# Optimization experiments

Hardware: AMD Instinct MI355X
Metric: run time of the kernel (lower is better)

The kernel has to match this reference:

```python
import jax, jax.numpy as jnp
import numpy as np

T = 100          # number of landscape sample points
K_MAX = 2        # landscape depth
GRID = (256, 256)
N = GRID[0] * GRID[1]
B = 256          # batch size
P = 1024         # persistence pairs per sample (from the cubical complex)
DIMENSIONS = (0, 1)
BIG = jnp.float32(1e30)  # finite sentinel instead of inf (avoids inf arithmetic)


def setup_inputs() -> dict:
    key = jax.random.key(0)
    k1, k2, k3, k4 = jax.random.split(key, 4)
    inputs = jax.random.uniform(k1, (B, N), dtype=jnp.float32)
    dim_idx = jax.random.randint(k2, (B, P), 0, 2, dtype=jnp.int32)
    b_loc = jax.random.randint(k3, (B, P), 0, N, dtype=jnp.int32)
    d_loc = jax.random.randint(k4, (B, P), 0, N, dtype=jnp.int32)
    # persistence pairs satisfy death value >= birth value; swap to honor that
    vb = jnp.take_along_axis(inputs, b_loc, axis=1)
    vd = jnp.take_along_axis(inputs, d_loc, axis=1)
    swap = vb > vd
    birth_loc = jnp.where(swap, d_loc, b_loc)
    death_loc = jnp.where(swap, b_loc, d_loc)
    return {"inputs": inputs, "dim_idx": dim_idx,
            "birth_loc": birth_loc, "death_loc": death_loc}


def _landscape_sample(dtm, dim_idx, b_loc, d_loc):
    # dtm: [N] filtration values; pairs: [P] each
    births = dtm[b_loc]  # [P] birth value = input at birth cell
    deaths = dtm[d_loc]  # [P]
    lands, trange = [], []
    for dim in DIMENSIONS:
        valid = dim_idx == dim                     # [P] pairs of this homology dim
        count = jnp.sum(valid)
        # robust t-range: first K_MAX valid pairs in given (lexsort) order
        rank = jnp.cumsum(valid.astype(jnp.int32)) - 1
        sel = valid & (rank < K_MAX)
        t_min = jnp.min(jnp.where(sel, births, BIG))
        t_max = jnp.max(jnp.where(sel, deaths, -BIG))
        t_min = jnp.where(count > 0, t_min, 0.0)
        t_max = jnp.where(count > 0, t_max, 0.0)
        # original custom grad does NOT differentiate through tseq
        tseq = jax.lax.stop_gradient(jnp.linspace(t_min, t_max, T))  # [T]
        b = jnp.where(valid, births, BIG)
        d = jnp.where(valid, deaths, -BIG)
        # tent functions: [T, P]
        fab = jnp.maximum(jnp.minimum(tseq[:, None] - b[None, :],
                                      d[None, :] - tseq[:, None]), 0.0)
        land, _ = jax.lax.top_k(fab, K_MAX)        # == -sort(-fab)[:, :K_MAX]
        land = jnp.where(count > 0, land, jnp.zeros_like(land))
        nonzero = (count > 0) & (jnp.max(land) > 0)
        trange.append(jnp.where(nonzero, t_min, 0.0))
        trange.append(jnp.where(nonzero, t_max, 0.0))
        lands.append(land)
    return jnp.stack(lands), jax.lax.stop_gradient(jnp.stack(trange))


def reference(inputs, dim_idx, birth_loc, death_loc):
    # landscape: [B, len(DIMENSIONS), T, K_MAX]; t_range: [B, 2*len(DIMENSIONS)]
    land, t_range = jax.vmap(_landscape_sample)(inputs, dim_idx, birth_loc, death_loc)
    return land, t_range
```

## Files before the change

### kernel.cpp

```cpp
#include <hip/hip_runtime.h>

#define TT 100
#define PP 1024
#define NN 65536
#define BIGV 1e30f

__global__ __launch_bounds__(1024, 8) void adpl_kernel(
    const float* __restrict__ inputs,
    const int*   __restrict__ dim_idx,
    const int*   __restrict__ birth_loc,
    const int*   __restrict__ death_loc,
    float*       __restrict__ out_land,
    float*       __restrict__ out_trange)
{
    __shared__ float2 bd[PP];
    __shared__ unsigned long long s_mask[16];
    __shared__ float  s_tmin, s_tmax;
    __shared__ int    s_count;
    __shared__ int    s_maxland;
    __shared__ float2 s_part[TT][33];

    const int b   = blockIdx.x;
    const int d   = blockIdx.y;
    const int tid = threadIdx.x;

    if (tid == 0) s_maxland = 0;

    {
        const int p  = tid;
        const int di = dim_idx[(size_t)b * PP + p];
        const bool v = (di == d);
        float bv = BIGV, dv = -BIGV;
        if (v) {
            const int bl = birth_loc[(size_t)b * PP + p];
            const int dl = death_loc[(size_t)b * PP + p];
            bv = inputs[(size_t)b * NN + bl];
            dv = inputs[(size_t)b * NN + dl];
        }
        bd[p] = make_float2(bv, dv);
        const unsigned long long m = __ballot(v);
        if ((tid & 63) == 0) s_mask[tid >> 6] = m;
    }
    __syncthreads();

    if (tid == 0) {
        int cnt = 0, p1 = -1, p2 = -1;
        for (int w = 0; w < 16; w++) {
            unsigned long long m = s_mask[w];
            cnt += __popcll(m);
            if (p2 < 0 && m) {
                if (p1 < 0) {
                    p1 = w * 64 + __ffsll(m) - 1;
                    m &= m - 1;
                    if (m) p2 = w * 64 + __ffsll(m) - 1;
                } else {
                    p2 = w * 64 + __ffsll(m) - 1;
                }
            }
        }
        float tmin = 0.f, tmax = 0.f;
        if (cnt > 0) {
            const float2 e1 = bd[p1];
            tmin = e1.x; tmax = e1.y;
            if (cnt > 1) {
                const float2 e2 = bd[p2];
                tmin = fminf(tmin, e2.x);
                tmax = fmaxf(tmax, e2.y);
            }
        }
        s_tmin = tmin; s_tmax = tmax; s_count = cnt;
    }
    __syncthreads();

    if (tid < 800) {
        const int tg = tid >> 5;
        const int c  = tid & 31;
        const float tmin = s_tmin, tmax = s_tmax;
        const float step = (tmax - tmin) * (1.0f / (TT - 1));
        float tv[4], m1[4], m2[4];
        #pragma unroll
        for (int j = 0; j < 4; j++) {
            const int t = 4 * tg + j;
            tv[j] = (t == TT - 1) ? tmax : fmaf((float)t, step, tmin);
            m1[j] = 0.f; m2[j] = 0.f;
        }
        #pragma unroll 8
        for (int i = 0; i < 32; i++) {
            const float2 e = bd[32 * i + c];
            #pragma unroll
            for (int j = 0; j < 4; j++) {
                const float f = fminf(tv[j] - e.x, e.y - tv[j]);
                m2[j] = fmaxf(m2[j], fminf(m1[j], f));
                m1[j] = fmaxf(m1[j], f);
            }
        }
        #pragma unroll
        for (int j = 0; j < 4; j++)
            s_part[4 * tg + j][c] = make_float2(m1[j], m2[j]);
    }
    __syncthreads();

    if (tid < TT) {
        const int t = tid;
        float m1 = 0.f, m2 = 0.f;
        #pragma unroll 8
        for (int c = 0; c < 32; c++) {
            const float2 pr = s_part[t][c];
            m2 = fmaxf(fminf(m1, pr.x), fmaxf(m2, pr.y));
            m1 = fmaxf(m1, pr.x);
        }
        const size_t base = ((size_t)(b * 2 + d) * TT + t) * 2;
        *reinterpret_cast<float2*>(out_land + base) = make_float2(m1, m2);
        atomicMax(&s_maxland, __float_as_int(m1));
    }
    __syncthreads();

    if (tid == 0) {
        const bool nz = (s_count > 0) && (__int_as_float(s_maxland) > 0.f);
        const float tmn = nz ? s_tmin : 0.f;
        const float tmx = nz ? s_tmax : 0.f;
        *reinterpret_cast<float2*>(out_trange + (size_t)b * 4 + 2 * d) =
            make_float2(tmn, tmx);
    }
}

extern "C" void kernel_launch(void* const* d_in, const int* in_sizes, int n_in,
                              void* d_out, int out_size, void* d_ws, size_t ws_size,
                              hipStream_t stream) {
    const float* inputs    = (const float*)d_in[0];
    const int*   dim_idx   = (const int*)d_in[1];
    const int*   birth_loc = (const int*)d_in[2];
    const int*   death_loc = (const int*)d_in[3];

    const int B = in_sizes[1] / PP;

    float* out_land   = (float*)d_out;
    float* out_trange = out_land + (size_t)B * 2 * TT * 2;

    dim3 grid(B, 2);
    adpl_kernel<<<grid, 1024, 0, stream>>>(inputs, dim_idx, birth_loc, death_loc,
                                           out_land, out_trange);
}
```

Before: 106.6 us.

## Compact valid pairs in shared memory and scan only the valid count

```diff
diff --git a/kernel.cpp b/kernel.cpp
--- a/kernel.cpp
+++ b/kernel.cpp
@@ -13,69 +13,62 @@
     float*       __restrict__ out_land,
     float*       __restrict__ out_trange)
 {
-    __shared__ float2 bd[PP];
+    __shared__ float2 bd[PP + 32];
     __shared__ unsigned long long s_mask[16];
-    __shared__ float  s_tmin, s_tmax;
-    __shared__ int    s_count;
+    __shared__ float2 s_part[TT][33];
     __shared__ int    s_maxland;
-    __shared__ float2 s_part[TT][33];
 
-    const int b   = blockIdx.x;
-    const int d   = blockIdx.y;
-    const int tid = threadIdx.x;
+    const int b    = blockIdx.x;
+    const int d    = blockIdx.y;
+    const int tid  = threadIdx.x;
+    const int wave = tid >> 6;
+    const int lane = tid & 63;
 
     if (tid == 0) s_maxland = 0;
 
-    {
-        const int p  = tid;
-        const int di = dim_idx[(size_t)b * PP + p];
-        const bool v = (di == d);
-        float bv = BIGV, dv = -BIGV;
-        if (v) {
-            const int bl = birth_loc[(size_t)b * PP + p];
-            const int dl = death_loc[(size_t)b * PP + p];
-            bv = inputs[(size_t)b * NN + bl];
-            dv = inputs[(size_t)b * NN + dl];
-        }
-        bd[p] = make_float2(bv, dv);
-        const unsigned long long m = __ballot(v);
-        if ((tid & 63) == 0) s_mask[tid >> 6] = m;
+    const int di = dim_idx  [(size_t)b * PP + tid];
+    const int bl = birth_loc[(size_t)b * PP + tid];
+    const int dl = death_loc[(size_t)b * PP + tid];
+    const bool v = (di == d);
+    float bv = 0.f, dv = 0.f;
+    if (v) {
+        bv = inputs[(size_t)b * NN + bl];
+        dv = inputs[(size_t)b * NN + dl];
     }
+    const unsigned long long m = __ballot(v);
+    if (lane == 0) s_mask[wave] = m;
     __syncthreads();
 
-    if (tid == 0) {
-        int cnt = 0, p1 = -1, p2 = -1;
-        for (int w = 0; w < 16; w++) {
-            unsigned long long m = s_mask[w];
-            cnt += __popcll(m);
-            if (p2 < 0 && m) {
-                if (p1 < 0) {
-                    p1 = w * 64 + __ffsll(m) - 1;
-                    m &= m - 1;
-                    if (m) p2 = w * 64 + __ffsll(m) - 1;
-                } else {
-                    p2 = w * 64 + __ffsll(m) - 1;
-                }
-            }
+    int cnt = 0, base = 0;
+    #pragma unroll
+    for (int w = 0; w < 16; w++) {
+        const int pc = __popcll(s_mask[w]);
+        cnt  += pc;
+        base += (w < wave) ? pc : 0;
+    }
+    if (v) {
+        const int prefix = __popcll(m & ((1ull << lane) - 1ull));
+        bd[base + prefix] = make_float2(bv, dv);
+    }
+    const int cnt_pad = (cnt + 31) & ~31;
+    if (tid < cnt_pad - cnt)
+        bd[cnt + tid] = make_float2(BIGV, -BIGV);
+    __syncthreads();
+
+    float tmin = 0.f, tmax = 0.f;
+    if (cnt > 0) {
+        const float2 e1 = bd[0];
+        tmin = e1.x; tmax = e1.y;
+        if (cnt > 1) {
+            const float2 e2 = bd[1];
+            tmin = fminf(tmin, e2.x);
+            tmax = fmaxf(tmax, e2.y);
         }
-        float tmin = 0.f, tmax = 0.f;
-        if (cnt > 0) {
-            const float2 e1 = bd[p1];
-            tmin = e1.x; tmax = e1.y;
-            if (cnt > 1) {
-                const float2 e2 = bd[p2];
-                tmin = fminf(tmin, e2.x);
-                tmax = fmaxf(tmax, e2.y);
-            }
-        }
-        s_tmin = tmin; s_tmax = tmax; s_count = cnt;
     }
-    __syncthreads();
 
     if (tid < 800) {
         const int tg = tid >> 5;
         const int c  = tid & 31;
-        const float tmin = s_tmin, tmax = s_tmax;
         const float step = (tmax - tmin) * (1.0f / (TT - 1));
         float tv[4], m1[4], m2[4];
         #pragma unroll
@@ -84,13 +77,14 @@
             tv[j] = (t == TT - 1) ? tmax : fmaf((float)t, step, tmin);
             m1[j] = 0.f; m2[j] = 0.f;
         }
-        #pragma unroll 8
-        for (int i = 0; i < 32; i++) {
-            const float2 e = bd[32 * i + c];
+        const int iters = cnt_pad >> 5;
+        #pragma unroll 4
+        for (int i = 0; i < iters; i++) {
+            const float2 e = bd[(i << 5) + c];
             #pragma unroll
             for (int j = 0; j < 4; j++) {
                 const float f = fminf(tv[j] - e.x, e.y - tv[j]);
-                m2[j] = fmaxf(m2[j], fminf(m1[j], f));
+                m2[j] = __builtin_amdgcn_fmed3f(m1[j], m2[j], f);
                 m1[j] = fmaxf(m1[j], f);
             }
         }
@@ -102,25 +96,23 @@
 
     if (tid < TT) {
         const int t = tid;
-        float m1 = 0.f, m2 = 0.f;
+        float M1 = 0.f, M2 = 0.f;
         #pragma unroll 8
         for (int c = 0; c < 32; c++) {
             const float2 pr = s_part[t][c];
-            m2 = fmaxf(fminf(m1, pr.x), fmaxf(m2, pr.y));
-            m1 = fmaxf(m1, pr.x);
+            M2 = __builtin_amdgcn_fmed3f(M1, pr.x, fmaxf(M2, pr.y));
+            M1 = fmaxf(M1, pr.x);
         }
-        const size_t base = ((size_t)(b * 2 + d) * TT + t) * 2;
-        *reinterpret_cast<float2*>(out_land + base) = make_float2(m1, m2);
-        atomicMax(&s_maxland, __float_as_int(m1));
+        const size_t base_o = ((size_t)(b * 2 + d) * TT + t) * 2;
+        *reinterpret_cast<float2*>(out_land + base_o) = make_float2(M1, M2);
+        atomicMax(&s_maxland, __float_as_int(M1));
     }
     __syncthreads();
 
     if (tid == 0) {
-        const bool nz = (s_count > 0) && (__int_as_float(s_maxland) > 0.f);
-        const float tmn = nz ? s_tmin : 0.f;
-        const float tmx = nz ? s_tmax : 0.f;
+        const bool nz = (cnt > 0) && (__int_as_float(s_maxland) > 0.f);
         *reinterpret_cast<float2*>(out_trange + (size_t)b * 4 + 2 * d) =
-            make_float2(tmn, tmx);
+            make_float2(nz ? tmin : 0.f, nz ? tmax : 0.f);
     }
 }
 
```

New measurement: 103.1 us. 1.03x faster.
